# Performance work log

Measured on AMD Instinct MI355X. Metric: run time of the kernel, lower is better.

The kernel has to match this reference:

```python
import jax, jax.numpy as jnp
import numpy as np

# CIN config: input_dim (num_fields) = 32, cross_layer_sizes = [128, 128, 128], split_half = True
NUM_FIELDS = 32
EMBED_DIM = 16
BATCH = 4096
CROSS_SIZES = [128, 128, 128]


def setup_inputs() -> dict:
    key = jax.random.key(0)
    ks = jax.random.split(key, 8)
    x = jax.random.normal(ks[0], (BATCH, NUM_FIELDS, EMBED_DIM), dtype=jnp.float32)
    # Conv1d(kernel_size=1) weights: (out_ch, in_ch) + bias (out_ch,)
    prev = NUM_FIELDS
    inp = {"x": x}
    for i, cs in enumerate(CROSS_SIZES):
        in_ch = NUM_FIELDS * prev
        scale = 1.0 / np.sqrt(in_ch)
        inp[f"W{i}"] = jax.random.uniform(ks[1 + 2 * i], (cs, in_ch), dtype=jnp.float32, minval=-scale, maxval=scale)
        inp[f"b{i}"] = jax.random.uniform(ks[2 + 2 * i], (cs,), dtype=jnp.float32, minval=-scale, maxval=scale)
        prev = cs // 2  # split_half (applied after all but last, but prev for next conv uses halved size)
    return inp


def _cin_forward(x, Ws, bs):
    # x: (B, F, E)
    x0 = x
    h = x
    xs = []
    n_layers = len(Ws)
    for i in range(n_layers):
        B, F, E = x0.shape
        G = h.shape[1]
        # outer product over field dims -> (B, F*G, E)
        z = (x0[:, :, None, :] * h[:, None, :, :]).reshape(B, F * G, E)
        # 1x1 conv == channel matmul; bias broadcast over embed dim; relu
        y = jax.nn.relu(jnp.einsum('oc,bce->boe', Ws[i], z) + bs[i][None, :, None])
        if i != n_layers - 1:
            half = y.shape[1] // 2
            x_keep, h = y[:, :half, :], y[:, half:, :]
        else:
            x_keep, h = y, y
        xs.append(x_keep)
    return jnp.sum(jnp.concatenate(xs, axis=1), axis=2)  # (B, fc_input_dim)


def reference(x, W0, b0, W1, b1, W2, b2):
    return _cin_forward(x, [W0, W1, W2], [b0, b1, b2])
```

## Files before the change

kernel.cpp:

```cpp
#include <hip/hip_runtime.h>

typedef _Float16 half_t;
typedef _Float16 v8h __attribute__((ext_vector_type(8)));
typedef float v4f __attribute__((ext_vector_type(4)));

#define XTP 40
#define HP  72

typedef __attribute__((address_space(3))) unsigned int lds_u32;
typedef const __attribute__((address_space(1))) unsigned int glb_u32;

__device__ __forceinline__ void dma16(const half_t* g, half_t* l, int lane) {
  __builtin_amdgcn_global_load_lds((glb_u32*)(g + lane * 8), (lds_u32*)(l), 16, 0, 0);
}

#define WAITVM(N) __builtin_amdgcn_s_waitcnt(0xF70 | (N))
#define SCHED0()  __builtin_amdgcn_sched_barrier(0)

__global__ __launch_bounds__(256) void prep_w_all(const float* __restrict__ W0,
                                                  const float* __restrict__ W1,
                                                  const float* __restrict__ W2,
                                                  half_t* __restrict__ w0h,
                                                  half_t* __restrict__ w1h,
                                                  half_t* __restrict__ w2h) {
  int i = blockIdx.x * 256 + threadIdx.x;
  const float* src; half_t* dst; int ktot; int j;
  if (i < 16384)      { src = W0; dst = w0h; ktot = 1024; j = i; }
  else if (i < 49152) { src = W1; dst = w1h; ktot = 2048; j = i - 16384; }
  else                { src = W2; dst = w2h; ktot = 2048; j = i - 49152; }
  int o = j & 127, k8 = j >> 7;
  const float* s = src + (size_t)o * ktot + k8 * 8;
  float4 f0 = *(const float4*)s;
  float4 f1 = *(const float4*)(s + 4);
  union { half_t h[8]; uint4 u; } pk;
  pk.h[0] = (half_t)f0.x; pk.h[1] = (half_t)f0.y; pk.h[2] = (half_t)f0.z; pk.h[3] = (half_t)f0.w;
  pk.h[4] = (half_t)f1.x; pk.h[5] = (half_t)f1.y; pk.h[6] = (half_t)f1.z; pk.h[7] = (half_t)f1.w;
  *(uint4*)(dst + (size_t)j * 8) = pk.u;
}

template <int G, int KTOT, int KEEP, int OUT_BASE, bool H_OUT, bool H_IS_X>
__device__ __forceinline__ void layer(const half_t* __restrict__ wgt,
                                      const float* __restrict__ bias,
                                      half_t* __restrict__ xt_lds,
                                      half_t* __restrict__ h_lds,
                                      half_t* __restrict__ w_ring,
                                      float* __restrict__ out,
                                      size_t b0, int tid, int phase) {
  constexpr int SPO = (G == 64) ? 16 : 8;
  constexpr int NOCT = (KTOT / 32) / SPO;
  constexpr int NSEL = (G == 64) ? 2 : 1;
  const int lane = tid & 63;
  const int wv = tid >> 6;
  const int wm = (wv & 1) * 64;
  const int wb = (wv >> 1) * 2;
  const int col = lane & 15;
  const int kq = lane >> 4;

  int lrow[2];
#pragma unroll
  for (int ni = 0; ni < 2; ++ni) lrow[ni] = (wb + ni) * 16 + col;

  __syncthreads();

  const half_t* hb = H_IS_X ? xt_lds : h_lds;
  const int hpitch = H_IS_X ? XTP : HP;
  v8h hreg[2][NSEL];
#pragma unroll
  for (int ni = 0; ni < 2; ++ni) {
    const half_t* hp = hb + lrow[ni] * hpitch + kq * 8;
    hreg[ni][0] = *(const v8h*)hp;
    if (NSEL > 1) hreg[ni][NSEL - 1] = *(const v8h*)(hp + 32);
  }

#pragma unroll
  for (int p = 0; p < 3; ++p) {
    const half_t* wsrc = wgt + (size_t)(phase * SPO + p) * 4096;
    dma16(wsrc + wv * 512, w_ring + p * 4096 + wv * 512, lane);
  }
  __syncthreads();

  v4f acc[4][2] = {};

#pragma unroll 1
  for (int oi = 0; oi < NOCT - 1; ++oi) {
    const int oct_a = (oi + phase) & 3;
    const int next_a = (oi + 1 + phase) & 3;
    v8h xv[2];
#pragma unroll
    for (int ni = 0; ni < 2; ++ni)
      xv[ni] = *(const v8h*)(xt_lds + lrow[ni] * XTP + oct_a * 8);
#pragma unroll
    for (int t = 0; t < SPO; ++t) {
      SCHED0(); WAITVM(2); __builtin_amdgcn_s_barrier(); SCHED0();
      {
        const int tp = t + 3;
        const half_t* wsrc = (tp < SPO)
            ? wgt + (size_t)(oct_a * SPO + tp) * 4096
            : wgt + (size_t)(next_a * SPO + (tp - SPO)) * 4096;
        dma16(wsrc + wv * 512, w_ring + (tp & 3) * 4096 + wv * 512, lane);
      }
      const half_t* rb = w_ring + (t & 3) * 4096;
      const int j = (G == 64) ? (t >> 1) : t;
      const int sel = (G == 64) ? (t & 1) : 0;
      v8h a[4], bfr[2];
#pragma unroll
      for (int mi = 0; mi < 4; ++mi)
        a[mi] = *(const v8h*)(rb + (kq * 128 + wm + mi * 16 + col) * 8);
#pragma unroll
      for (int ni = 0; ni < 2; ++ni)
        bfr[ni] = hreg[ni][sel] * xv[ni][j];
#pragma unroll
      for (int mi = 0; mi < 4; ++mi)
#pragma unroll
        for (int ni = 0; ni < 2; ++ni)
          acc[mi][ni] = __builtin_amdgcn_mfma_f32_16x16x32_f16(a[mi], bfr[ni], acc[mi][ni], 0, 0, 0);
    }
  }

  {
    const int oct_a = (NOCT - 1 + phase) & 3;
    v8h xv[2];
#pragma unroll
    for (int ni = 0; ni < 2; ++ni)
      xv[ni] = *(const v8h*)(xt_lds + lrow[ni] * XTP + oct_a * 8);
#pragma unroll
    for (int t = 0; t < SPO; ++t) {
      SCHED0();
      if (t < SPO - 2) { WAITVM(2); } else if (t == SPO - 2) { WAITVM(1); } else { WAITVM(0); }
      __builtin_amdgcn_s_barrier(); SCHED0();
      if (t + 3 < SPO) {
        const int tp = t + 3;
        const half_t* wsrc = wgt + (size_t)(oct_a * SPO + tp) * 4096;
        dma16(wsrc + wv * 512, w_ring + (tp & 3) * 4096 + wv * 512, lane);
      }
      const half_t* rb = w_ring + (t & 3) * 4096;
      const int j = (G == 64) ? (t >> 1) : t;
      const int sel = (G == 64) ? (t & 1) : 0;
      v8h a[4], bfr[2];
#pragma unroll
      for (int mi = 0; mi < 4; ++mi)
        a[mi] = *(const v8h*)(rb + (kq * 128 + wm + mi * 16 + col) * 8);
#pragma unroll
      for (int ni = 0; ni < 2; ++ni)
        bfr[ni] = hreg[ni][sel] * xv[ni][j];
#pragma unroll
      for (int mi = 0; mi < 4; ++mi)
#pragma unroll
        for (int ni = 0; ni < 2; ++ni)
          acc[mi][ni] = __builtin_amdgcn_mfma_f32_16x16x32_f16(a[mi], bfr[ni], acc[mi][ni], 0, 0, 0);
    }
  }

#pragma unroll
  for (int mi = 0; mi < 4; ++mi) {
    const int o_base = wm + mi * 16 + kq * 4;
    float4 b4 = *(const float4*)(bias + o_base);
#pragma unroll
    for (int ni = 0; ni < 2; ++ni) {
      const int bb = wb + ni;
      float v[4];
#pragma unroll
      for (int r = 0; r < 4; ++r)
        v[r] = fmaxf(acc[mi][ni][r] + (&b4.x)[r], 0.0f);
      if (H_OUT && o_base >= 64) {
        union { half_t h[4]; uint2 u; } pk;
#pragma unroll
        for (int r = 0; r < 4; ++r) pk.h[r] = (half_t)v[r];
        *(uint2*)(h_lds + (bb * 16 + col) * HP + (o_base - 64)) = pk.u;
      }
      if (o_base < KEEP) {
#pragma unroll
        for (int r = 0; r < 4; ++r) {
          float sv = v[r];
          sv += __shfl_xor(sv, 1);
          sv += __shfl_xor(sv, 2);
          sv += __shfl_xor(sv, 4);
          sv += __shfl_xor(sv, 8);
          if (col == 0) out[(b0 + bb) * 256 + OUT_BASE + o_base + r] = sv;
        }
      }
    }
  }
}

__global__ __launch_bounds__(512, 4) void cin_fused(const float* __restrict__ x,
                                                    const half_t* __restrict__ w0h,
                                                    const half_t* __restrict__ w1h,
                                                    const half_t* __restrict__ w2h,
                                                    const float* __restrict__ b0p,
                                                    const float* __restrict__ b1p,
                                                    const float* __restrict__ b2p,
                                                    float* __restrict__ out) {
  __shared__ __align__(16) half_t xt_lds[128 * XTP];
  __shared__ __align__(16) half_t h_lds[128 * HP];
  __shared__ __align__(16) half_t w_ring[4 * 4096];

  const int tid = threadIdx.x;
  const size_t b0 = (size_t)blockIdx.x * 8;
  const int phase = (blockIdx.x >> 3) & 3;

#pragma unroll
  for (int i = 0; i < 2; ++i) {
    int idx = (i * 512 + tid) * 4;
    float4 v = *(const float4*)(x + b0 * 512 + idx);
    int e = idx & 15, f = (idx >> 4) & 31, b = idx >> 9;
    half_t* d = xt_lds + (b * 16 + e) * XTP + f;
    d[0 * XTP] = (half_t)v.x;
    d[1 * XTP] = (half_t)v.y;
    d[2 * XTP] = (half_t)v.z;
    d[3 * XTP] = (half_t)v.w;
  }

  layer<32, 1024, 64, 0, true, true>(w0h, b0p, xt_lds, h_lds, w_ring, out, b0, tid, phase);
  layer<64, 2048, 64, 64, true, false>(w1h, b1p, xt_lds, h_lds, w_ring, out, b0, tid, phase);
  layer<64, 2048, 128, 128, false, false>(w2h, b2p, xt_lds, h_lds, w_ring, out, b0, tid, phase);
}

extern "C" void kernel_launch(void* const* d_in, const int* in_sizes, int n_in,
                              void* d_out, int out_size, void* d_ws, size_t ws_size,
                              hipStream_t stream) {
  const float* x  = (const float*)d_in[0];
  const float* W0 = (const float*)d_in[1];
  const float* b0 = (const float*)d_in[2];
  const float* W1 = (const float*)d_in[3];
  const float* b1 = (const float*)d_in[4];
  const float* W2 = (const float*)d_in[5];
  const float* b2 = (const float*)d_in[6];
  float* out = (float*)d_out;
  char* ws = (char*)d_ws;

  half_t* w0h = (half_t*)(ws);
  half_t* w1h = (half_t*)(ws + (256u << 10));
  half_t* w2h = (half_t*)(ws + (768u << 10));

  prep_w_all<<<320, 256, 0, stream>>>(W0, W1, W2, w0h, w1h, w2h);
  cin_fused<<<512, 512, 0, stream>>>(x, w0h, w1h, w2h, b0, b1, b2, out);
}
```

Baseline: 148.7 us.

## Retile CIN waves to 32x64 and stream weights in natural K order with rotating ring

Changes each wave's tile from 64 outputs x 2 batch groups to 32 outputs x 4 batch groups, so every wave loads 2 weight fragments per step instead of 4 while reusing them across 4 B operands. The weight repack now lays slices out in plain k order, and the per-block phase rotation is removed, so all blocks stream the weights in the same sequence. A rotating pointer ring replaces the modular ring indexing, and the initial prefetch no longer waits on a full syncthreads. The intent is to cut LDS read traffic per MFMA. In exchange, all blocks now hit the same weight addresses at the same time and each wave holds more hreg state.

```diff
diff --git a/kernel.cpp b/kernel.cpp
--- a/kernel.cpp
+++ b/kernel.cpp
@@ -2,6 +2,7 @@
 
 typedef _Float16 half_t;
 typedef _Float16 v8h __attribute__((ext_vector_type(8)));
+typedef _Float16 v4h __attribute__((ext_vector_type(4)));
 typedef float v4f __attribute__((ext_vector_type(4)));
 
 #define XTP 40
@@ -24,18 +25,57 @@
                                                   half_t* __restrict__ w1h,
                                                   half_t* __restrict__ w2h) {
   int i = blockIdx.x * 256 + threadIdx.x;
-  const float* src; half_t* dst; int ktot; int j;
-  if (i < 16384)      { src = W0; dst = w0h; ktot = 1024; j = i; }
-  else if (i < 49152) { src = W1; dst = w1h; ktot = 2048; j = i - 16384; }
-  else                { src = W2; dst = w2h; ktot = 2048; j = i - 49152; }
-  int o = j & 127, k8 = j >> 7;
+  const float* src; half_t* dst; int o, k8, ktot;
+  if (i < 16384)      { o = i >> 7;               k8 = i & 127;               src = W0; dst = w0h; ktot = 1024; }
+  else if (i < 49152) { int j = i - 16384; o = j >> 8; k8 = j & 255;          src = W1; dst = w1h; ktot = 2048; }
+  else                { int j = i - 49152; o = j >> 8; k8 = j & 255;          src = W2; dst = w2h; ktot = 2048; }
   const float* s = src + (size_t)o * ktot + k8 * 8;
   float4 f0 = *(const float4*)s;
   float4 f1 = *(const float4*)(s + 4);
   union { half_t h[8]; uint4 u; } pk;
   pk.h[0] = (half_t)f0.x; pk.h[1] = (half_t)f0.y; pk.h[2] = (half_t)f0.z; pk.h[3] = (half_t)f0.w;
   pk.h[4] = (half_t)f1.x; pk.h[5] = (half_t)f1.y; pk.h[6] = (half_t)f1.z; pk.h[7] = (half_t)f1.w;
-  *(uint4*)(dst + (size_t)j * 8) = pk.u;
+  *(uint4*)(dst + (size_t)(k8 * 128 + o) * 8) = pk.u;
+}
+
+template <int G, int NSEL, bool TAIL>
+__device__ __forceinline__ void run_quad(const half_t* __restrict__ wgt, int sbase,
+                                         half_t* (&r)[4], int wv, int lane, int arow,
+                                         const half_t* __restrict__ xt_lds, const int (&lrow)[4],
+                                         const v8h (&hreg)[4][NSEL], v4f (&acc)[2][4]) {
+  v8h xv8[4]; v4h xv4[4];
+  if (G == 64) {
+#pragma unroll
+    for (int ni = 0; ni < 4; ++ni) xv4[ni] = *(const v4h*)(xt_lds + lrow[ni] * XTP + (sbase >> 1));
+  } else {
+#pragma unroll
+    for (int ni = 0; ni < 4; ++ni) xv8[ni] = *(const v8h*)(xt_lds + lrow[ni] * XTP + sbase);
+  }
+#pragma unroll
+  for (int i = 0; i < 8; ++i) {
+    SCHED0();
+    if (!TAIL || i <= 5) { WAITVM(2); } else if (i == 6) { WAITVM(1); } else { WAITVM(0); }
+    __builtin_amdgcn_s_barrier();
+    SCHED0();
+    if (!TAIL || i <= 4)
+      dma16(wgt + (size_t)(sbase + i + 3) * 4096 + wv * 512, r[3] + wv * 512, lane);
+    const int sel = (G == 64) ? (i & 1) : 0;
+    v8h a0 = *(const v8h*)(r[0] + arow);
+    v8h a1 = *(const v8h*)(r[0] + arow + 128);
+    v8h bfr[4];
+#pragma unroll
+    for (int ni = 0; ni < 4; ++ni) {
+      half_t xs = (G == 64) ? xv4[ni][i >> 1] : xv8[ni][i];
+      bfr[ni] = hreg[ni][sel] * xs;
+    }
+#pragma unroll
+    for (int ni = 0; ni < 4; ++ni)
+      acc[0][ni] = __builtin_amdgcn_mfma_f32_16x16x32_f16(a0, bfr[ni], acc[0][ni], 0, 0, 0);
+#pragma unroll
+    for (int ni = 0; ni < 4; ++ni)
+      acc[1][ni] = __builtin_amdgcn_mfma_f32_16x16x32_f16(a1, bfr[ni], acc[1][ni], 0, 0, 0);
+    half_t* t = r[0]; r[0] = r[1]; r[1] = r[2]; r[2] = r[3]; r[3] = t;
+  }
 }
 
 template <int G, int KTOT, int KEEP, int OUT_BASE, bool H_OUT, bool H_IS_X>
@@ -45,138 +85,72 @@
                                       half_t* __restrict__ h_lds,
                                       half_t* __restrict__ w_ring,
                                       float* __restrict__ out,
-                                      size_t b0, int tid, int phase) {
-  constexpr int SPO = (G == 64) ? 16 : 8;
-  constexpr int NOCT = (KTOT / 32) / SPO;
+                                      size_t b0, int tid) {
+  constexpr int NS = KTOT / 32;
+  constexpr int NQ = NS / 8;
   constexpr int NSEL = (G == 64) ? 2 : 1;
   const int lane = tid & 63;
   const int wv = tid >> 6;
-  const int wm = (wv & 1) * 64;
-  const int wb = (wv >> 1) * 2;
+  const int wm = (wv & 3) * 32;
+  const int wb = (wv >> 2) * 4;
   const int col = lane & 15;
   const int kq = lane >> 4;
-
-  int lrow[2];
-#pragma unroll
-  for (int ni = 0; ni < 2; ++ni) lrow[ni] = (wb + ni) * 16 + col;
+  const int arow = (kq * 128 + wm + col) * 8;
+
+  int lrow[4];
+#pragma unroll
+  for (int ni = 0; ni < 4; ++ni) lrow[ni] = (wb + ni) * 16 + col;
 
   __syncthreads();
 
   const half_t* hb = H_IS_X ? xt_lds : h_lds;
   const int hpitch = H_IS_X ? XTP : HP;
-  v8h hreg[2][NSEL];
-#pragma unroll
-  for (int ni = 0; ni < 2; ++ni) {
+  v8h hreg[4][NSEL];
+#pragma unroll
+  for (int ni = 0; ni < 4; ++ni) {
     const half_t* hp = hb + lrow[ni] * hpitch + kq * 8;
     hreg[ni][0] = *(const v8h*)hp;
     if (NSEL > 1) hreg[ni][NSEL - 1] = *(const v8h*)(hp + 32);
   }
 
 #pragma unroll
-  for (int p = 0; p < 3; ++p) {
-    const half_t* wsrc = wgt + (size_t)(phase * SPO + p) * 4096;
-    dma16(wsrc + wv * 512, w_ring + p * 4096 + wv * 512, lane);
-  }
-  __syncthreads();
-
-  v4f acc[4][2] = {};
+  for (int p = 0; p < 3; ++p)
+    dma16(wgt + (size_t)p * 4096 + wv * 512, w_ring + p * 4096 + wv * 512, lane);
+
+  half_t* r[4] = {w_ring, w_ring + 4096, w_ring + 8192, w_ring + 12288};
+  v4f acc[2][4] = {};
 
 #pragma unroll 1
-  for (int oi = 0; oi < NOCT - 1; ++oi) {
-    const int oct_a = (oi + phase) & 3;
-    const int next_a = (oi + 1 + phase) & 3;
-    v8h xv[2];
-#pragma unroll
-    for (int ni = 0; ni < 2; ++ni)
-      xv[ni] = *(const v8h*)(xt_lds + lrow[ni] * XTP + oct_a * 8);
-#pragma unroll
-    for (int t = 0; t < SPO; ++t) {
-      SCHED0(); WAITVM(2); __builtin_amdgcn_s_barrier(); SCHED0();
-      {
-        const int tp = t + 3;
-        const half_t* wsrc = (tp < SPO)
-            ? wgt + (size_t)(oct_a * SPO + tp) * 4096
-            : wgt + (size_t)(next_a * SPO + (tp - SPO)) * 4096;
-        dma16(wsrc + wv * 512, w_ring + (tp & 3) * 4096 + wv * 512, lane);
-      }
-      const half_t* rb = w_ring + (t & 3) * 4096;
-      const int j = (G == 64) ? (t >> 1) : t;
-      const int sel = (G == 64) ? (t & 1) : 0;
-      v8h a[4], bfr[2];
-#pragma unroll
-      for (int mi = 0; mi < 4; ++mi)
-        a[mi] = *(const v8h*)(rb + (kq * 128 + wm + mi * 16 + col) * 8);
-#pragma unroll
-      for (int ni = 0; ni < 2; ++ni)
-        bfr[ni] = hreg[ni][sel] * xv[ni][j];
-#pragma unroll
-      for (int mi = 0; mi < 4; ++mi)
-#pragma unroll
-        for (int ni = 0; ni < 2; ++ni)
-          acc[mi][ni] = __builtin_amdgcn_mfma_f32_16x16x32_f16(a[mi], bfr[ni], acc[mi][ni], 0, 0, 0);
-    }
-  }
-
-  {
-    const int oct_a = (NOCT - 1 + phase) & 3;
-    v8h xv[2];
-#pragma unroll
-    for (int ni = 0; ni < 2; ++ni)
-      xv[ni] = *(const v8h*)(xt_lds + lrow[ni] * XTP + oct_a * 8);
-#pragma unroll
-    for (int t = 0; t < SPO; ++t) {
-      SCHED0();
-      if (t < SPO - 2) { WAITVM(2); } else if (t == SPO - 2) { WAITVM(1); } else { WAITVM(0); }
-      __builtin_amdgcn_s_barrier(); SCHED0();
-      if (t + 3 < SPO) {
-        const int tp = t + 3;
-        const half_t* wsrc = wgt + (size_t)(oct_a * SPO + tp) * 4096;
-        dma16(wsrc + wv * 512, w_ring + (tp & 3) * 4096 + wv * 512, lane);
-      }
-      const half_t* rb = w_ring + (t & 3) * 4096;
-      const int j = (G == 64) ? (t >> 1) : t;
-      const int sel = (G == 64) ? (t & 1) : 0;
-      v8h a[4], bfr[2];
-#pragma unroll
-      for (int mi = 0; mi < 4; ++mi)
-        a[mi] = *(const v8h*)(rb + (kq * 128 + wm + mi * 16 + col) * 8);
-#pragma unroll
-      for (int ni = 0; ni < 2; ++ni)
-        bfr[ni] = hreg[ni][sel] * xv[ni][j];
-#pragma unroll
-      for (int mi = 0; mi < 4; ++mi)
-#pragma unroll
-        for (int ni = 0; ni < 2; ++ni)
-          acc[mi][ni] = __builtin_amdgcn_mfma_f32_16x16x32_f16(a[mi], bfr[ni], acc[mi][ni], 0, 0, 0);
-    }
-  }
-
-#pragma unroll
-  for (int mi = 0; mi < 4; ++mi) {
+  for (int q = 0; q < NQ - 1; ++q)
+    run_quad<G, NSEL, false>(wgt, q * 8, r, wv, lane, arow, xt_lds, lrow, hreg, acc);
+  run_quad<G, NSEL, true>(wgt, (NQ - 1) * 8, r, wv, lane, arow, xt_lds, lrow, hreg, acc);
+
+#pragma unroll
+  for (int mi = 0; mi < 2; ++mi) {
     const int o_base = wm + mi * 16 + kq * 4;
     float4 b4 = *(const float4*)(bias + o_base);
 #pragma unroll
-    for (int ni = 0; ni < 2; ++ni) {
+    for (int ni = 0; ni < 4; ++ni) {
       const int bb = wb + ni;
       float v[4];
 #pragma unroll
-      for (int r = 0; r < 4; ++r)
-        v[r] = fmaxf(acc[mi][ni][r] + (&b4.x)[r], 0.0f);
+      for (int r2 = 0; r2 < 4; ++r2)
+        v[r2] = fmaxf(acc[mi][ni][r2] + (&b4.x)[r2], 0.0f);
       if (H_OUT && o_base >= 64) {
         union { half_t h[4]; uint2 u; } pk;
 #pragma unroll
-        for (int r = 0; r < 4; ++r) pk.h[r] = (half_t)v[r];
+        for (int r2 = 0; r2 < 4; ++r2) pk.h[r2] = (half_t)v[r2];
         *(uint2*)(h_lds + (bb * 16 + col) * HP + (o_base - 64)) = pk.u;
       }
       if (o_base < KEEP) {
 #pragma unroll
-        for (int r = 0; r < 4; ++r) {
-          float sv = v[r];
+        for (int r2 = 0; r2 < 4; ++r2) {
+          float sv = v[r2];
           sv += __shfl_xor(sv, 1);
           sv += __shfl_xor(sv, 2);
           sv += __shfl_xor(sv, 4);
           sv += __shfl_xor(sv, 8);
-          if (col == 0) out[(b0 + bb) * 256 + OUT_BASE + o_base + r] = sv;
+          if (col == 0) out[(b0 + bb) * 256 + OUT_BASE + o_base + r2] = sv;
         }
       }
     }
@@ -197,7 +171,6 @@
 
   const int tid = threadIdx.x;
   const size_t b0 = (size_t)blockIdx.x * 8;
-  const int phase = (blockIdx.x >> 3) & 3;
 
 #pragma unroll
   for (int i = 0; i < 2; ++i) {
@@ -211,9 +184,9 @@
     d[3 * XTP] = (half_t)v.w;
   }
 
-  layer<32, 1024, 64, 0, true, true>(w0h, b0p, xt_lds, h_lds, w_ring, out, b0, tid, phase);
-  layer<64, 2048, 64, 64, true, false>(w1h, b1p, xt_lds, h_lds, w_ring, out, b0, tid, phase);
-  layer<64, 2048, 128, 128, false, false>(w2h, b2p, xt_lds, h_lds, w_ring, out, b0, tid, phase);
+  layer<32, 1024, 64, 0, true, true>(w0h, b0p, xt_lds, h_lds, w_ring, out, b0, tid);
+  layer<64, 2048, 64, 64, true, false>(w1h, b1p, xt_lds, h_lds, w_ring, out, b0, tid);
+  layer<64, 2048, 128, 128, false, false>(w2h, b2p, xt_lds, h_lds, w_ring, out, b0, tid);
 }
 
 extern "C" void kernel_launch(void* const* d_in, const int* in_sizes, int n_in,
```

Measured after the change: 153.1 us. +3.0%, slower.
